# Kernel tuning notes

Measured on AMD Instinct MI355X. Metric: run time of the kernel, lower is better.

Reference implementation:

```python
import jax, jax.numpy as jnp
import numpy as np

B, C, P, D = 16, 16, 512, 256

def setup_inputs() -> dict:
    key = jax.random.key(0)
    ks = jax.random.split(key, 5)
    return {
        "query": jax.random.normal(ks[0], (B, C, P, D), dtype=jnp.float32),
        "attn_weight": jax.random.normal(ks[1], (C, P, D), dtype=jnp.float32) * (1.0 / np.sqrt(D)),
        "q_proj_weight": jax.random.normal(ks[2], (C, D, D), dtype=jnp.float32) * (1.0 / np.sqrt(D)),
        "k_proj_weight": jax.random.normal(ks[3], (C, D, D), dtype=jnp.float32) * (1.0 / np.sqrt(D)),
        "v_proj_weight": jax.random.normal(ks[4], (C, D, D), dtype=jnp.float32) * (1.0 / np.sqrt(D)),
        "q_proj_bias": jnp.zeros((C, 1, D), dtype=jnp.float32),
        "k_proj_bias": jnp.zeros((C, 1, D), dtype=jnp.float32),
        "v_proj_bias": jnp.zeros((C, 1, D), dtype=jnp.float32),
    }

def reference(query, attn_weight, q_proj_weight, k_proj_weight, v_proj_weight,
              q_proj_bias, k_proj_bias, v_proj_bias):
    d = query.shape[-1]
    # cross-cycle context: sum over cycles minus own contribution
    acw = attn_weight * query                      # (B,C,P,D)
    context = acw.sum(axis=-3, keepdims=True) - acw  # (B,C,P,D)
    # per-cycle batched projections with ReLU
    q = jax.nn.relu(jnp.einsum('bcpd,cde->bcpe', query, q_proj_weight) + q_proj_bias)
    k = jax.nn.relu(jnp.einsum('bcpd,cde->bcpe', context, k_proj_weight) + k_proj_bias)
    v = jax.nn.relu(jnp.einsum('bcpd,cde->bcpe', context, v_proj_weight) + v_proj_bias)
    q = q * (float(d) ** -0.5)
    scores = jnp.einsum('bcpe,bcqe->bcpq', q, k)   # (B,C,P,P)
    attn = jax.nn.softmax(scores, axis=-1)         # dropout p=0.0 -> identity
    out = jnp.einsum('bcpq,bcqe->bcpe', attn, v)   # (B,C,P,D)
    return out
```

## Files before the change

### kernel.cpp

```cpp
#include <hip/hip_runtime.h>
#include <math.h>

#define B_ 16
#define C_ 16
#define P_ 512
#define D_ 256

constexpr int HEADS = B_ * C_;
constexpr int PD    = P_ * D_;
constexpr float QSCALE = 0.0625f;

typedef __attribute__((ext_vector_type(8))) short short8;
typedef __attribute__((ext_vector_type(4))) short short4_t;
typedef __attribute__((ext_vector_type(4))) float floatx4;

#define MFMA_BF16 __builtin_amdgcn_mfma_f32_16x16x32_bf16

__device__ inline short2 split_hl(float x) {
    unsigned xb = __float_as_uint(x);
    unsigned hb = (xb + 0x8000u) & 0xFFFF0000u;
    float lf = x - __uint_as_float(hb);
    short2 r;
    r.x = (short)(hb >> 16);
    r.y = (short)((__float_as_uint(lf) + 0x8000u) >> 16);
    return r;
}
__device__ inline unsigned packsplit(float x) {
    short2 s = split_hl(x);
    return (unsigned)(unsigned short)s.x | ((unsigned)(unsigned short)s.y << 16);
}

__device__ inline void gload16(const unsigned* g, unsigned* l) {
    __builtin_amdgcn_global_load_lds(
        (__attribute__((address_space(1))) void*)(g),
        (__attribute__((address_space(3))) void*)(l), 16, 0, 0);
}

__device__ inline void stage_sw(const unsigned* __restrict__ g, int gstride,
                                unsigned* lds, int tid) {
    int wv = tid >> 6, lane = tid & 63;
    int rsub = lane >> 3, slot = lane & 7;
#pragma unroll
    for (int it = 0; it < 4; ++it) {
        int r0 = it * 32 + wv * 8;
        int row = r0 + rsub;
        const unsigned* src = g + (size_t)row * gstride + ((slot ^ (row & 7)) << 2);
        gload16(src, &lds[r0 * 32]);
    }
}

__device__ inline void stage_sw8(const unsigned* __restrict__ g, int gstride,
                                 unsigned* lds, int tid) {
    int wv = tid >> 6, lane = tid & 63;
    int rsub = lane >> 3, slot = lane & 7;
#pragma unroll
    for (int it = 0; it < 2; ++it) {
        int r0 = it * 64 + wv * 8;
        int row = r0 + rsub;
        const unsigned* src = g + (size_t)row * gstride + ((slot ^ (row & 7)) << 2);
        gload16(src, &lds[r0 * 32]);
    }
}

__device__ inline void unpack8(const uint4& a, const uint4& b, short8& h, short8& l) {
    union { unsigned u[4]; short8 s; } H, L;
    H.u[0] = __builtin_amdgcn_perm(a.y, a.x, 0x05040100u);
    L.u[0] = __builtin_amdgcn_perm(a.y, a.x, 0x07060302u);
    H.u[1] = __builtin_amdgcn_perm(a.w, a.z, 0x05040100u);
    L.u[1] = __builtin_amdgcn_perm(a.w, a.z, 0x07060302u);
    H.u[2] = __builtin_amdgcn_perm(b.y, b.x, 0x05040100u);
    L.u[2] = __builtin_amdgcn_perm(b.y, b.x, 0x07060302u);
    H.u[3] = __builtin_amdgcn_perm(b.w, b.z, 0x05040100u);
    L.u[3] = __builtin_amdgcn_perm(b.w, b.z, 0x07060302u);
    h = H.s; l = L.s;
}

__device__ inline void rdfrag_sw(const unsigned* lds, int r, int hi,
                                 short8& h, short8& l) {
    int base = r * 32;
    int x = r & 7;
    const uint4 a = *reinterpret_cast<const uint4*>(&lds[base + ((((hi << 1))     ^ x) << 2)]);
    const uint4 b = *reinterpret_cast<const uint4*>(&lds[base + ((((hi << 1) | 1) ^ x) << 2)]);
    unpack8(a, b, h, l);
}

__device__ inline void rdfrag_pad(const unsigned* lds, int r, int hi,
                                  short8& h, short8& l) {
    const uint4 a = *reinterpret_cast<const uint4*>(&lds[r * 36 + hi * 8]);
    const uint4 b = *reinterpret_cast<const uint4*>(&lds[r * 36 + hi * 8 + 4]);
    unpack8(a, b, h, l);
}

__global__ __launch_bounds__(256) void k_sum_acw(const float* __restrict__ query,
                                                 const float* __restrict__ aw,
                                                 float* __restrict__ S) {
    int idx = blockIdx.x * 256 + threadIdx.x;
    int e = idx * 4;
    int d = e % D_;
    int p = (e / D_) % P_;
    int b = e / (D_ * P_);
    const float4* q4 = reinterpret_cast<const float4*>(query);
    const float4* a4 = reinterpret_cast<const float4*>(aw);
    int qbase = (((b * C_) * P_ + p) * D_ + d) >> 2;
    int abase = (p * D_ + d) >> 2;
    float4 acc = {0.f, 0.f, 0.f, 0.f};
#pragma unroll
    for (int c = 0; c < C_; ++c) {
        float4 qv = q4[qbase + c * (PD / 4)];
        float4 av = a4[abase + c * (PD / 4)];
        acc.x += qv.x * av.x;
        acc.y += qv.y * av.y;
        acc.z += qv.z * av.z;
        acc.w += qv.w * av.w;
    }
    reinterpret_cast<float4*>(S)[idx] = acc;
}

__global__ __launch_bounds__(256) void k_wpack(const float* __restrict__ Wq,
                                               const float* __restrict__ Wk,
                                               const float* __restrict__ Wv,
                                               unsigned* __restrict__ W2t) {
    __shared__ float tile[64][68];
    int wsel = blockIdx.z / C_;
    int c    = blockIdx.z % C_;
    int k0 = blockIdx.x * 64, n0 = blockIdx.y * 64;
    const float* Wsrc = wsel == 0 ? Wq : (wsel == 1 ? Wk : Wv);
    int tid = threadIdx.x;
#pragma unroll
    for (int it = 0; it < 4; ++it) {
        int idx = tid + it * 256;
        int kr = idx >> 4, nc = (idx & 15) * 4;
        float4 f = *reinterpret_cast<const float4*>(
            &Wsrc[(size_t)(c * D_ + k0 + kr) * D_ + n0 + nc]);
        *reinterpret_cast<float4*>(&tile[kr][nc]) = f;
    }
    __syncthreads();
#pragma unroll
    for (int it = 0; it < 4; ++it) {
        int idx = tid + it * 256;
        int nr = idx >> 4, kc = (idx & 15) * 4;
        uint4 u;
        u.x = packsplit(tile[kc + 0][nr]);
        u.y = packsplit(tile[kc + 1][nr]);
        u.z = packsplit(tile[kc + 2][nr]);
        u.w = packsplit(tile[kc + 3][nr]);
        *reinterpret_cast<uint4*>(
            &W2t[((size_t)(wsel * C_ + c) * D_ + n0 + nr) * D_ + k0 + kc]) = u;
    }
}

__global__ __launch_bounds__(256) void k_proj_mfma(
    const float* __restrict__ query, const float* __restrict__ aw,
    const float* __restrict__ S, const unsigned* __restrict__ W2t,
    const float* __restrict__ bq, const float* __restrict__ bk,
    const float* __restrict__ bv,
    unsigned* __restrict__ Q2, unsigned* __restrict__ K2,
    unsigned* __restrict__ V2t, int head0) {
    __shared__ unsigned Aw[2][128 * 36];
    __shared__ unsigned Bw[2][128 * 32];
    int tid = threadIdx.x;
    int lane = tid & 63, wv = tid >> 6;
    int wm = wv >> 1, wn = wv & 1;
    int ln = lane & 15, hi = lane >> 4, quad4 = hi * 4;
    int n0 = blockIdx.x * 128;
    int m0 = blockIdx.y * 128;
    int lh = blockIdx.z / 3, oid = blockIdx.z % 3;
    int hd = head0 + lh;
    int b = hd / C_, c = hd % C_;
    const unsigned* Wt = W2t + (size_t)(oid * C_ + c) * D_ * D_;

    int arow = tid >> 3, ack = (tid & 7) * 4;

    floatx4 acc[4][4] = {};

    stage_sw(Wt + (size_t)n0 * D_, D_, &Bw[0][0], tid);
#pragma unroll
    for (int it = 0; it < 4; ++it) {
        int row = arow + it * 32;
        float4 qv = *reinterpret_cast<const float4*>(
            &query[(size_t)(hd * P_ + m0 + row) * D_ + ack]);
        float x0, x1, x2, x3;
        if (oid == 0) {
            x0 = qv.x; x1 = qv.y; x2 = qv.z; x3 = qv.w;
        } else {
            float4 sv = *reinterpret_cast<const float4*>(
                &S[(size_t)(b * P_ + m0 + row) * D_ + ack]);
            float4 av = *reinterpret_cast<const float4*>(
                &aw[(size_t)(c * P_ + m0 + row) * D_ + ack]);
            x0 = sv.x - av.x * qv.x; x1 = sv.y - av.y * qv.y;
            x2 = sv.z - av.z * qv.z; x3 = sv.w - av.w * qv.w;
        }
        uint4 u;
        u.x = packsplit(x0); u.y = packsplit(x1);
        u.z = packsplit(x2); u.w = packsplit(x3);
        *reinterpret_cast<uint4*>(&Aw[0][row * 36 + ack]) = u;
    }
    __syncthreads();

    int cur = 0;
    for (int t = 0; t < 8; ++t) {
        int nx = cur ^ 1;
        bool pf = t < 7;
        int kk = (t + 1) * 32;
        if (pf) stage_sw(Wt + (size_t)n0 * D_ + kk, D_, &Bw[nx][0], tid);
        float4 qv[4], sv[4], av[4];
        if (pf) {
#pragma unroll
            for (int it = 0; it < 4; ++it) {
                int row = arow + it * 32;
                qv[it] = *reinterpret_cast<const float4*>(
                    &query[(size_t)(hd * P_ + m0 + row) * D_ + kk + ack]);
                if (oid != 0) {
                    sv[it] = *reinterpret_cast<const float4*>(
                        &S[(size_t)(b * P_ + m0 + row) * D_ + kk + ack]);
                    av[it] = *reinterpret_cast<const float4*>(
                        &aw[(size_t)(c * P_ + m0 + row) * D_ + kk + ack]);
                }
            }
        }
        short8 ah[4], alo[4], bh[4], blo[4];
#pragma unroll
        for (int i = 0; i < 4; ++i) {
            rdfrag_pad(&Aw[cur][0], wm * 64 + i * 16 + ln, hi, ah[i], alo[i]);
            rdfrag_sw(&Bw[cur][0], wn * 64 + i * 16 + ln, hi, bh[i], blo[i]);
        }
#pragma unroll
        for (int i = 0; i < 4; ++i)
#pragma unroll
            for (int j = 0; j < 4; ++j) {
                acc[i][j] = MFMA_BF16(ah[i], bh[j], acc[i][j], 0, 0, 0);
                acc[i][j] = MFMA_BF16(ah[i], blo[j], acc[i][j], 0, 0, 0);
                acc[i][j] = MFMA_BF16(alo[i], bh[j], acc[i][j], 0, 0, 0);
            }
        if (pf) {
#pragma unroll
            for (int it = 0; it < 4; ++it) {
                int row = arow + it * 32;
                float x0, x1, x2, x3;
                if (oid == 0) {
                    x0 = qv[it].x; x1 = qv[it].y; x2 = qv[it].z; x3 = qv[it].w;
                } else {
                    x0 = sv[it].x - av[it].x * qv[it].x;
                    x1 = sv[it].y - av[it].y * qv[it].y;
                    x2 = sv[it].z - av[it].z * qv[it].z;
                    x3 = sv[it].w - av[it].w * qv[it].w;
                }
                uint4 u;
                u.x = packsplit(x0); u.y = packsplit(x1);
                u.z = packsplit(x2); u.w = packsplit(x3);
                *reinterpret_cast<uint4*>(&Aw[nx][row * 36 + ack]) = u;
            }
        }
        __syncthreads();
        cur = nx;
    }

    const float* bias = oid == 0 ? bq : (oid == 1 ? bk : bv);
    float scale = oid == 0 ? QSCALE : 1.0f;
#pragma unroll
    for (int j = 0; j < 4; ++j) {
        int n_g = n0 + wn * 64 + j * 16 + ln;
        float bb = bias[c * D_ + n_g];
#pragma unroll
        for (int i = 0; i < 4; ++i) {
            int p0 = m0 + wm * 64 + i * 16 + quad4;
            if (oid == 2) {
                uint4 u;
                u.x = packsplit(fmaxf(acc[i][j][0] + bb, 0.f));
                u.y = packsplit(fmaxf(acc[i][j][1] + bb, 0.f));
                u.z = packsplit(fmaxf(acc[i][j][2] + bb, 0.f));
                u.w = packsplit(fmaxf(acc[i][j][3] + bb, 0.f));
                *reinterpret_cast<uint4*>(&V2t[(size_t)(lh * D_ + n_g) * P_ + p0]) = u;
            } else {
                unsigned* dst = oid == 0 ? Q2 : K2;
#pragma unroll
                for (int r = 0; r < 4; ++r) {
                    float v = fmaxf(acc[i][j][r] + bb, 0.f) * scale;
                    dst[(size_t)(lh * P_ + p0 + r) * D_ + n_g] = packsplit(v);
                }
            }
        }
    }
}

__global__ __launch_bounds__(512) void k_attn(
    const unsigned* __restrict__ Q2, const unsigned* __restrict__ K2,
    const unsigned* __restrict__ V2t, float* __restrict__ O, int head0) {
    __shared__ unsigned chunk[4][128 * 32];
    __shared__ unsigned Pl[8][16 * 128];
    int tid = threadIdx.x;
    int lane = tid & 63, wv = tid >> 6;
    int ln = lane & 15, hi = lane >> 4;
    int lh = blockIdx.x;
    int m0 = blockIdx.y * 128;
    int hd = head0 + lh;
    const unsigned* gq = Q2 + ((size_t)lh * P_ + m0) * D_;
    const unsigned* gk = K2 + (size_t)lh * P_ * D_;
    const unsigned* gv = V2t + (size_t)lh * D_ * P_;
    unsigned* myP = &Pl[wv][0];

    floatx4 o[16] = {};
    float m_[4], l_[4];
#pragma unroll
    for (int r = 0; r < 4; ++r) { m_[r] = -INFINITY; l_[r] = 0.f; }

    stage_sw8(gq, D_, chunk[0], tid);
    stage_sw8(gk, D_, chunk[2], tid);
    __syncthreads();
    int cur = 0;

    for (int kv = 0; kv < 4; ++kv) {
        floatx4 s_[8] = {};
        for (int kk = 0; kk < 8; ++kk) {
            int nx = cur ^ 1;
            if (kk < 7) {
                stage_sw8(gq + (kk + 1) * 32, D_, chunk[nx], tid);
                stage_sw8(gk + (size_t)(kv * 128) * D_ + (kk + 1) * 32, D_,
                          chunk[2 + nx], tid);
            } else {
                stage_sw8(gv + kv * 128, P_, chunk[nx], tid);
                stage_sw8(gv + (size_t)128 * P_ + kv * 128, P_, chunk[2 + nx], tid);
            }
            short8 ah, al_, bh, bl_;
            rdfrag_sw(chunk[cur], wv * 16 + ln, hi, ah, al_);
            __builtin_amdgcn_s_setprio(1);
#pragma unroll
            for (int j = 0; j < 8; ++j) {
                rdfrag_sw(chunk[2 + cur], j * 16 + ln, hi, bh, bl_);
                s_[j] = MFMA_BF16(ah, bh, s_[j], 0, 0, 0);
                s_[j] = MFMA_BF16(ah, bl_, s_[j], 0, 0, 0);
                s_[j] = MFMA_BF16(al_, bh, s_[j], 0, 0, 0);
            }
            __builtin_amdgcn_s_setprio(0);
            __syncthreads();
            cur = nx;
        }

        float sc[4], rs[4];
#pragma unroll
        for (int r = 0; r < 4; ++r) {
            float mx = s_[0][r];
#pragma unroll
            for (int j = 1; j < 8; ++j) mx = fmaxf(mx, s_[j][r]);
            mx = fmaxf(mx, __shfl_xor(mx, 1));
            mx = fmaxf(mx, __shfl_xor(mx, 2));
            mx = fmaxf(mx, __shfl_xor(mx, 4));
            mx = fmaxf(mx, __shfl_xor(mx, 8));
            float mn = fmaxf(m_[r], mx);
            sc[r] = __expf(m_[r] - mn);
            m_[r] = mn;
            rs[r] = 0.f;
        }
#pragma unroll
        for (int n = 0; n < 16; ++n)
#pragma unroll
            for (int r = 0; r < 4; ++r) o[n][r] *= sc[r];

#pragma unroll
        for (int j = 0; j < 8; ++j)
#pragma unroll
            for (int r = 0; r < 4; ++r) {
                float p = __expf(s_[j][r] - m_[r]);
                rs[r] += p;
                int row = hi * 4 + r, col = j * 16 + ln;
                int slot = (col >> 2) ^ (row & 7);
                myP[row * 128 + slot * 4 + (col & 3)] = packsplit(p);
            }
#pragma unroll
        for (int r = 0; r < 4; ++r) {
            float s = rs[r];
            s += __shfl_xor(s, 1);
            s += __shfl_xor(s, 2);
            s += __shfl_xor(s, 4);
            s += __shfl_xor(s, 8);
            l_[r] = l_[r] * sc[r] + s;
        }

        for (int kq = 0; kq < 4; ++kq) {
            int nx = cur ^ 1;
            if (kq < 3) {
                stage_sw8(gv + kv * 128 + (kq + 1) * 32, P_, chunk[nx], tid);
                stage_sw8(gv + (size_t)128 * P_ + kv * 128 + (kq + 1) * 32, P_,
                          chunk[2 + nx], tid);
            } else if (kv < 3) {
                stage_sw8(gq, D_, chunk[nx], tid);
                stage_sw8(gk + (size_t)((kv + 1) * 128) * D_, D_, chunk[2 + nx], tid);
            }
            int x = ln & 7;
            const uint4 a0 = *reinterpret_cast<const uint4*>(
                &myP[ln * 128 + (((kq * 8 + 2 * hi)) ^ x) * 4]);
            const uint4 a1 = *reinterpret_cast<const uint4*>(
                &myP[ln * 128 + (((kq * 8 + 2 * hi + 1)) ^ x) * 4]);
            short8 pah, pal;
            unpack8(a0, a1, pah, pal);
            __builtin_amdgcn_s_setprio(1);
#pragma unroll
            for (int n = 0; n < 16; ++n) {
                short8 vh, vl;
                const unsigned* vb = (n < 8) ? chunk[cur] : chunk[2 + cur];
                rdfrag_sw(vb, (n & 7) * 16 + ln, hi, vh, vl);
                o[n] = MFMA_BF16(pah, vh, o[n], 0, 0, 0);
                o[n] = MFMA_BF16(pah, vl, o[n], 0, 0, 0);
                o[n] = MFMA_BF16(pal, vh, o[n], 0, 0, 0);
            }
            __builtin_amdgcn_s_setprio(0);
            __syncthreads();
            cur = nx;
        }
    }

    float inv[4];
#pragma unroll
    for (int r = 0; r < 4; ++r) inv[r] = 1.0f / l_[r];
#pragma unroll
    for (int n = 0; n < 16; ++n) {
        int col = n * 16 + ln;
#pragma unroll
        for (int r = 0; r < 4; ++r) {
            int row = m0 + wv * 16 + hi * 4 + r;
            O[((size_t)hd * P_ + row) * D_ + col] = o[n][r] * inv[r];
        }
    }
}

extern "C" void kernel_launch(void* const* d_in, const int* in_sizes, int n_in,
                              void* d_out, int out_size, void* d_ws, size_t ws_size,
                              hipStream_t stream) {
    (void)in_sizes; (void)n_in; (void)out_size;
    const float* query = (const float*)d_in[0];
    const float* aw    = (const float*)d_in[1];
    const float* Wq    = (const float*)d_in[2];
    const float* Wk    = (const float*)d_in[3];
    const float* Wv    = (const float*)d_in[4];
    const float* bq    = (const float*)d_in[5];
    const float* bk    = (const float*)d_in[6];
    const float* bv    = (const float*)d_in[7];
    float* out = (float*)d_out;

    char* ws = (char*)d_ws;
    const size_t s_words   = (size_t)B_ * P_ * D_;
    const size_t w2t_words = (size_t)3 * C_ * D_ * D_;
    const size_t fixed_bytes = (s_words + w2t_words) * 4;
    const size_t per_head_bytes = (size_t)3 * P_ * D_ * 4;
    size_t avail = ws_size > fixed_bytes ? ws_size - fixed_bytes : 0;
    int H = (int)(avail / per_head_bytes);
    if (H < 1) H = 1;
    if (H > HEADS) H = HEADS;

    float*    S   = (float*)ws;
    unsigned* W2t = (unsigned*)(ws + s_words * 4);
    unsigned* Q2  = (unsigned*)(ws + fixed_bytes);
    unsigned* K2  = Q2 + (size_t)H * P_ * D_;
    unsigned* V2t = K2 + (size_t)H * P_ * D_;

    k_sum_acw<<<(B_ * P_ * D_ / 4) / 256, 256, 0, stream>>>(query, aw, S);
    k_wpack<<<dim3(D_ / 64, D_ / 64, 3 * C_), 256, 0, stream>>>(Wq, Wk, Wv, W2t);

    for (int head0 = 0; head0 < HEADS; head0 += H) {
        int Hc = HEADS - head0 < H ? HEADS - head0 : H;
        k_proj_mfma<<<dim3(D_ / 128, P_ / 128, 3 * Hc), 256, 0, stream>>>(
            query, aw, S, W2t, bq, bk, bv, Q2, K2, V2t, head0);
        k_attn<<<dim3(Hc, P_ / 128), 512, 0, stream>>>(Q2, K2, V2t, out, head0);
    }
}
```

Baseline: 919.1 us.

## Compute transposed scores to keep softmax probabilities in registers, drop P LDS round-trip

The QK^T MFMA now computes S^T (K as A operand, Q as B), so each lane holds a column of probabilities that maps directly onto the A-operand layout for the PV MFMA. The per-wave LDS buffer for P and its write/read/unpack are removed, the V staging uses a permuted slot order to match, and row statistics are reduced with cross-half shuffles and broadcast back via __shfl. LDS rows get padding every 8 rows, and the launch bounds request 4 blocks per CU. This trades LDS traffic and footprint for more register pressure, since the P fragments are held in registers, and a tighter occupancy target that may force spills.

```diff
diff --git a/kernel.cpp b/kernel.cpp
--- a/kernel.cpp
+++ b/kernel.cpp
@@ -9,6 +9,7 @@
 constexpr int HEADS = B_ * C_;
 constexpr int PD    = P_ * D_;
 constexpr float QSCALE = 0.0625f;
+constexpr int CHW = 128 * 32 + 16 * 4;
 
 typedef __attribute__((ext_vector_type(8))) short short8;
 typedef __attribute__((ext_vector_type(4))) short short4_t;
@@ -35,6 +36,7 @@
         (__attribute__((address_space(1))) void*)(g),
         (__attribute__((address_space(3))) void*)(l), 16, 0, 0);
 }
+__device__ inline int ldsrow(int r) { return r * 32 + ((r >> 3) << 2); }
 
 __device__ inline void stage_sw(const unsigned* __restrict__ g, int gstride,
                                 unsigned* lds, int tid) {
@@ -45,7 +47,7 @@
         int r0 = it * 32 + wv * 8;
         int row = r0 + rsub;
         const unsigned* src = g + (size_t)row * gstride + ((slot ^ (row & 7)) << 2);
-        gload16(src, &lds[r0 * 32]);
+        gload16(src, &lds[ldsrow(r0)]);
     }
 }
 
@@ -58,7 +60,22 @@
         int r0 = it * 64 + wv * 8;
         int row = r0 + rsub;
         const unsigned* src = g + (size_t)row * gstride + ((slot ^ (row & 7)) << 2);
-        gload16(src, &lds[r0 * 32]);
+        gload16(src, &lds[ldsrow(r0)]);
+    }
+}
+
+__device__ inline void stage_sw8_v(const unsigned* __restrict__ g, int gstride,
+                                   unsigned* lds, int tid) {
+    int wv = tid >> 6, lane = tid & 63;
+    int rsub = lane >> 3, slot = lane & 7;
+#pragma unroll
+    for (int it = 0; it < 2; ++it) {
+        int r0 = it * 64 + wv * 8;
+        int row = r0 + rsub;
+        int sg = slot ^ (row & 7);
+        sg = ((sg & 1) << 2) | (sg >> 1);
+        const unsigned* src = g + (size_t)row * gstride + (sg << 2);
+        gload16(src, &lds[ldsrow(r0)]);
     }
 }
 
@@ -77,7 +94,7 @@
 
 __device__ inline void rdfrag_sw(const unsigned* lds, int r, int hi,
                                  short8& h, short8& l) {
-    int base = r * 32;
+    int base = ldsrow(r);
     int x = r & 7;
     const uint4 a = *reinterpret_cast<const uint4*>(&lds[base + ((((hi << 1))     ^ x) << 2)]);
     const uint4 b = *reinterpret_cast<const uint4*>(&lds[base + ((((hi << 1) | 1) ^ x) << 2)]);
@@ -157,7 +174,7 @@
     unsigned* __restrict__ Q2, unsigned* __restrict__ K2,
     unsigned* __restrict__ V2t, int head0) {
     __shared__ unsigned Aw[2][128 * 36];
-    __shared__ unsigned Bw[2][128 * 32];
+    __shared__ unsigned Bw[2][CHW];
     int tid = threadIdx.x;
     int lane = tid & 63, wv = tid >> 6;
     int wm = wv >> 1, wn = wv & 1;
@@ -283,11 +300,10 @@
     }
 }
 
-__global__ __launch_bounds__(512) void k_attn(
+__global__ __launch_bounds__(512, 4) void k_attn(
     const unsigned* __restrict__ Q2, const unsigned* __restrict__ K2,
     const unsigned* __restrict__ V2t, float* __restrict__ O, int head0) {
-    __shared__ unsigned chunk[4][128 * 32];
-    __shared__ unsigned Pl[8][16 * 128];
+    __shared__ unsigned chunk[4][CHW];
     int tid = threadIdx.x;
     int lane = tid & 63, wv = tid >> 6;
     int ln = lane & 15, hi = lane >> 4;
@@ -297,12 +313,9 @@
     const unsigned* gq = Q2 + ((size_t)lh * P_ + m0) * D_;
     const unsigned* gk = K2 + (size_t)lh * P_ * D_;
     const unsigned* gv = V2t + (size_t)lh * D_ * P_;
-    unsigned* myP = &Pl[wv][0];
 
     floatx4 o[16] = {};
-    float m_[4], l_[4];
-#pragma unroll
-    for (int r = 0; r < 4; ++r) { m_[r] = -INFINITY; l_[r] = 0.f; }
+    float m_ = -INFINITY, l_ = 0.f;
 
     stage_sw8(gq, D_, chunk[0], tid);
     stage_sw8(gk, D_, chunk[2], tid);
@@ -318,90 +331,81 @@
                 stage_sw8(gk + (size_t)(kv * 128) * D_ + (kk + 1) * 32, D_,
                           chunk[2 + nx], tid);
             } else {
-                stage_sw8(gv + kv * 128, P_, chunk[nx], tid);
-                stage_sw8(gv + (size_t)128 * P_ + kv * 128, P_, chunk[2 + nx], tid);
-            }
-            short8 ah, al_, bh, bl_;
-            rdfrag_sw(chunk[cur], wv * 16 + ln, hi, ah, al_);
+                stage_sw8_v(gv + kv * 128, P_, chunk[nx], tid);
+                stage_sw8_v(gv + (size_t)128 * P_ + kv * 128, P_, chunk[2 + nx], tid);
+            }
+            short8 qh, ql, kh, kl;
+            rdfrag_sw(chunk[cur], wv * 16 + ln, hi, qh, ql);
             __builtin_amdgcn_s_setprio(1);
 #pragma unroll
             for (int j = 0; j < 8; ++j) {
-                rdfrag_sw(chunk[2 + cur], j * 16 + ln, hi, bh, bl_);
-                s_[j] = MFMA_BF16(ah, bh, s_[j], 0, 0, 0);
-                s_[j] = MFMA_BF16(ah, bl_, s_[j], 0, 0, 0);
-                s_[j] = MFMA_BF16(al_, bh, s_[j], 0, 0, 0);
+                rdfrag_sw(chunk[2 + cur], j * 16 + ln, hi, kh, kl);
+                s_[j] = MFMA_BF16(kh, qh, s_[j], 0, 0, 0);
+                s_[j] = MFMA_BF16(kh, ql, s_[j], 0, 0, 0);
+                s_[j] = MFMA_BF16(kl, qh, s_[j], 0, 0, 0);
             }
             __builtin_amdgcn_s_setprio(0);
             __syncthreads();
             cur = nx;
         }
 
-        float sc[4], rs[4];
-#pragma unroll
-        for (int r = 0; r < 4; ++r) {
-            float mx = s_[0][r];
-#pragma unroll
-            for (int j = 1; j < 8; ++j) mx = fmaxf(mx, s_[j][r]);
-            mx = fmaxf(mx, __shfl_xor(mx, 1));
-            mx = fmaxf(mx, __shfl_xor(mx, 2));
-            mx = fmaxf(mx, __shfl_xor(mx, 4));
-            mx = fmaxf(mx, __shfl_xor(mx, 8));
-            float mn = fmaxf(m_[r], mx);
-            sc[r] = __expf(m_[r] - mn);
-            m_[r] = mn;
-            rs[r] = 0.f;
-        }
+        float mx = s_[0][0];
+#pragma unroll
+        for (int j = 0; j < 8; ++j)
+#pragma unroll
+            for (int r = 0; r < 4; ++r) mx = fmaxf(mx, s_[j][r]);
+        mx = fmaxf(mx, __shfl_xor(mx, 16));
+        mx = fmaxf(mx, __shfl_xor(mx, 32));
+        float mn = fmaxf(m_, mx);
+        float sc = __expf(m_ - mn);
+        m_ = mn;
+
+        float rs = 0.f;
+        short8 pah[4], pal[4];
+#pragma unroll
+        for (int kq = 0; kq < 4; ++kq)
+#pragma unroll
+            for (int t = 0; t < 4; ++t) {
+                float pa = __expf(s_[2 * kq][t] - m_);
+                float pb = __expf(s_[2 * kq + 1][t] - m_);
+                rs += pa + pb;
+                short2 sa = split_hl(pa), sb = split_hl(pb);
+                pah[kq][t] = sa.x;     pal[kq][t] = sa.y;
+                pah[kq][4 + t] = sb.x; pal[kq][4 + t] = sb.y;
+            }
+        rs += __shfl_xor(rs, 16);
+        rs += __shfl_xor(rs, 32);
+        l_ = l_ * sc + rs;
+
+        float scr[4];
+#pragma unroll
+        for (int r = 0; r < 4; ++r)
+            scr[r] = __shfl(sc, (lane & 48) | (hi * 4 + r));
 #pragma unroll
         for (int n = 0; n < 16; ++n)
 #pragma unroll
-            for (int r = 0; r < 4; ++r) o[n][r] *= sc[r];
-
-#pragma unroll
-        for (int j = 0; j < 8; ++j)
-#pragma unroll
-            for (int r = 0; r < 4; ++r) {
-                float p = __expf(s_[j][r] - m_[r]);
-                rs[r] += p;
-                int row = hi * 4 + r, col = j * 16 + ln;
-                int slot = (col >> 2) ^ (row & 7);
-                myP[row * 128 + slot * 4 + (col & 3)] = packsplit(p);
-            }
-#pragma unroll
-        for (int r = 0; r < 4; ++r) {
-            float s = rs[r];
-            s += __shfl_xor(s, 1);
-            s += __shfl_xor(s, 2);
-            s += __shfl_xor(s, 4);
-            s += __shfl_xor(s, 8);
-            l_[r] = l_[r] * sc[r] + s;
-        }
-
+            for (int r = 0; r < 4; ++r) o[n][r] *= scr[r];
+
+#pragma unroll
         for (int kq = 0; kq < 4; ++kq) {
             int nx = cur ^ 1;
             if (kq < 3) {
-                stage_sw8(gv + kv * 128 + (kq + 1) * 32, P_, chunk[nx], tid);
-                stage_sw8(gv + (size_t)128 * P_ + kv * 128 + (kq + 1) * 32, P_,
-                          chunk[2 + nx], tid);
+                stage_sw8_v(gv + kv * 128 + (kq + 1) * 32, P_, chunk[nx], tid);
+                stage_sw8_v(gv + (size_t)128 * P_ + kv * 128 + (kq + 1) * 32, P_,
+                            chunk[2 + nx], tid);
             } else if (kv < 3) {
                 stage_sw8(gq, D_, chunk[nx], tid);
                 stage_sw8(gk + (size_t)((kv + 1) * 128) * D_, D_, chunk[2 + nx], tid);
             }
-            int x = ln & 7;
-            const uint4 a0 = *reinterpret_cast<const uint4*>(
-                &myP[ln * 128 + (((kq * 8 + 2 * hi)) ^ x) * 4]);
-            const uint4 a1 = *reinterpret_cast<const uint4*>(
-                &myP[ln * 128 + (((kq * 8 + 2 * hi + 1)) ^ x) * 4]);
-            short8 pah, pal;
-            unpack8(a0, a1, pah, pal);
             __builtin_amdgcn_s_setprio(1);
 #pragma unroll
             for (int n = 0; n < 16; ++n) {
                 short8 vh, vl;
                 const unsigned* vb = (n < 8) ? chunk[cur] : chunk[2 + cur];
                 rdfrag_sw(vb, (n & 7) * 16 + ln, hi, vh, vl);
-                o[n] = MFMA_BF16(pah, vh, o[n], 0, 0, 0);
-                o[n] = MFMA_BF16(pah, vl, o[n], 0, 0, 0);
-                o[n] = MFMA_BF16(pal, vh, o[n], 0, 0, 0);
+                o[n] = MFMA_BF16(pah[kq], vh, o[n], 0, 0, 0);
+                o[n] = MFMA_BF16(pah[kq], vl, o[n], 0, 0, 0);
+                o[n] = MFMA_BF16(pal[kq], vh, o[n], 0, 0, 0);
             }
             __builtin_amdgcn_s_setprio(0);
             __syncthreads();
@@ -409,16 +413,18 @@
         }
     }
 
-    float inv[4];
-#pragma unroll
-    for (int r = 0; r < 4; ++r) inv[r] = 1.0f / l_[r];
+    float inv = 1.0f / l_;
+    float invr[4];
+#pragma unroll
+    for (int r = 0; r < 4; ++r)
+        invr[r] = __shfl(inv, (lane & 48) | (hi * 4 + r));
 #pragma unroll
     for (int n = 0; n < 16; ++n) {
         int col = n * 16 + ln;
 #pragma unroll
         for (int r = 0; r < 4; ++r) {
             int row = m0 + wv * 16 + hi * 4 + r;
-            O[((size_t)hd * P_ + row) * D_ + col] = o[n][r] * inv[r];
+            O[((size_t)hd * P_ + row) * D_ + col] = o[n][r] * invr[r];
         }
     }
 }
```

Result: slower. 1.372 ms (+49.3%).
